# Kernel optimization log

Measured on AMD Instinct MI355X. Metric: run time of the kernel, lower is better.

## Reference

```python
import jax, jax.numpy as jnp
import numpy as np

NUM_CATEGORIES = 64
IN_DIM = 1024
OUT_DIM = 1024
BATCH = 32
SEQ = 512


def setup_inputs() -> dict:
    key = jax.random.key(0)
    k1, k2, k3 = jax.random.split(key, 3)
    x = jax.random.normal(k1, (BATCH, SEQ, IN_DIM), dtype=jnp.float32)
    category_ids = jax.random.randint(k2, (BATCH,), 0, NUM_CATEGORIES, dtype=jnp.int32)
    weight = (jax.random.normal(k3, (NUM_CATEGORIES, IN_DIM, OUT_DIM), dtype=jnp.float32) * 0.02)
    bias = jnp.zeros((NUM_CATEGORIES, OUT_DIM), dtype=jnp.float32)
    return {"x": x, "category_ids": category_ids, "weight": weight, "bias": bias}


def reference(x, category_ids, weight, bias):
    # Gather per-sample weights/biases: W [b, in, out], b [b, out]
    W = weight[category_ids]
    b = bias[category_ids]
    # x: [b, l, in] -> out: [b, l, out]
    return jnp.einsum('bli,bio->blo', x, W) + b[:, None, :]
```

## Files before the change

kernel.cpp:

```cpp
#include <hip/hip_runtime.h>
#include <type_traits>

#define NUM_CATEGORIES 64
#define IN_DIM 1024
#define OUT_DIM 1024
#define BATCH 32
#define SEQ 512

#define BM 256
#define BN 256
#define BK 32
#define NSTEP (IN_DIM / BK)

#define LDA 40
#define LDBW 260

typedef float f32x4 __attribute__((ext_vector_type(4)));
typedef float f32x2 __attribute__((ext_vector_type(2)));
typedef unsigned int u32x4 __attribute__((ext_vector_type(4)));
typedef __bf16 bf16x2 __attribute__((ext_vector_type(2)));
typedef __bf16 bf16x4 __attribute__((ext_vector_type(4)));
typedef __bf16 bf16x8 __attribute__((ext_vector_type(8)));

__global__ __launch_bounds__(512, 2)
void cslinear_kernel(const float* __restrict__ x,
                     const int* __restrict__ cid,
                     const float* __restrict__ weight,
                     const float* __restrict__ bias,
                     float* __restrict__ out) {
    __shared__ unsigned short As[2][BM * LDA];
    __shared__ unsigned int   Bs[2][(BK / 2) * LDBW];

    const int t    = threadIdx.x;
    const int lane = t & 63;
    const int w    = t >> 6;

    const int s    = blockIdx.x;
    const int xcd  = s & 7;
    const int ixd  = s >> 3;
    const int b    = xcd + 8 * (ixd >> 3);
    const int j    = ixd & 7;
    const int nt   = j & 3;
    const int mt   = j >> 2;

    const int c = cid[b];
    const float* Wp = weight + (size_t)c * IN_DIM * OUT_DIM + (size_t)nt * BN;
    const float* Xp = x + ((size_t)b * SEQ + (size_t)mt * BM) * IN_DIM;
    float* Op = out + ((size_t)b * SEQ + (size_t)mt * BM) * OUT_DIM + (size_t)nt * BN;

    f32x4 acc[8][4] = {};

    const int mbase = (w >> 2) * 128;
    const int nbase = (w & 3) * 64;
    const int lrow  = lane & 15;
    const int lhi   = lane >> 4;

    f32x4 ra[2][4];
    f32x4 rb0[2][2], rb1[2][2];

    auto LOAD_A = [&](int ks, auto S) {
        constexpr int ss = decltype(S)::value;
        const float* Xk = Xp + ks * BK;
        #pragma unroll
        for (int i = 0; i < 4; ++i) {
            int f   = i * 512 + t;
            int row = f >> 3;
            int c4  = f & 7;
            ra[ss][i] = *reinterpret_cast<const f32x4*>(Xk + (size_t)row * IN_DIM + c4 * 4);
        }
    };
    auto LOAD_B = [&](int ks, auto S) {
        constexpr int ss = decltype(S)::value;
        const float* Wk = Wp + (size_t)(ks * BK) * OUT_DIM;
        #pragma unroll
        for (int i = 0; i < 2; ++i) {
            int u  = i * 512 + t;
            int kp = u >> 6;
            int n4 = u & 63;
            const float* bse = Wk + (size_t)(2 * kp) * OUT_DIM + n4 * 4;
            rb0[ss][i] = *reinterpret_cast<const f32x4*>(bse);
            rb1[ss][i] = *reinterpret_cast<const f32x4*>(bse + OUT_DIM);
        }
    };

    auto ST_A = [&](auto S, auto I) {
        constexpr int ss = decltype(S)::value;
        constexpr int i  = decltype(I)::value;
        char* AsB = reinterpret_cast<char*>(&As[ss][0]);
        int f   = i * 512 + t;
        int row = f >> 3;
        int c4  = f & 7;
        bf16x4 a4 = __builtin_convertvector(ra[ss][i], bf16x4);
        *reinterpret_cast<bf16x4*>(AsB + row * (LDA * 2) + c4 * 8) = a4;
    };
    auto ST_B = [&](auto S, auto I) {
        constexpr int ss = decltype(S)::value;
        constexpr int i  = decltype(I)::value;
        unsigned int* BsW = &Bs[ss][0];
        int u  = i * 512 + t;
        int kp = u >> 6;
        int n4 = u & 63;
        u32x4 q;
        #pragma unroll
        for (int jj = 0; jj < 4; ++jj) {
            f32x2 pr;
            pr.x = rb0[ss][i][jj];
            pr.y = rb1[ss][i][jj];
            bf16x2 pb = __builtin_convertvector(pr, bf16x2);
            q[jj] = __builtin_bit_cast(unsigned int, pb);
        }
        *reinterpret_cast<u32x4*>(BsW + kp * LDBW + n4 * 4) = q;
    };

    constexpr std::integral_constant<int, 0> I0{};
    constexpr std::integral_constant<int, 1> I1{};
    constexpr std::integral_constant<int, 2> I2{};
    constexpr std::integral_constant<int, 3> I3{};
    constexpr std::integral_constant<int, 0> S0{};
    constexpr std::integral_constant<int, 1> S1{};

    auto CLUSTER = [&](auto S, auto Q, const bf16x8* bfr) {
        constexpr int ss = decltype(S)::value;
        constexpr int q  = decltype(Q)::value;
        const char* AsB = reinterpret_cast<const char*>(&As[ss][0]);
        __builtin_amdgcn_s_setprio(1);
        #pragma unroll
        for (int mi = q * 2; mi < q * 2 + 2; ++mi) {
            int r = mbase + mi * 16 + lrow;
            bf16x8 afr = *reinterpret_cast<const bf16x8*>(AsB + r * (LDA * 2) + lhi * 16);
            #pragma unroll
            for (int ni = 0; ni < 4; ++ni)
                acc[mi][ni] = __builtin_amdgcn_mfma_f32_16x16x32_bf16(
                    afr, bfr[ni], acc[mi][ni], 0, 0, 0);
        }
        __builtin_amdgcn_s_setprio(0);
    };

    auto REGION = [&](auto Sc, auto Sn, bool do_store, bool do_load, int ksl) {
        constexpr int sc = decltype(Sc)::value;
        const unsigned int* BsW = &Bs[sc][0];
        bf16x8 bfr[4];
        #pragma unroll
        for (int ni = 0; ni < 4; ++ni) {
            int n   = nbase + ni * 16 + lrow;
            int kp0 = lhi * 4;
            u32x4 wds;
            #pragma unroll
            for (int jj = 0; jj < 4; ++jj)
                wds[jj] = BsW[(kp0 + jj) * LDBW + n];
            bfr[ni] = __builtin_bit_cast(bf16x8, wds);
        }
        CLUSTER(Sc, I0, bfr);
        if (do_store) { ST_A(Sn, I0); ST_A(Sn, I1); }
        CLUSTER(Sc, I1, bfr);
        if (do_store) { ST_A(Sn, I2); ST_A(Sn, I3); }
        if (do_load)  LOAD_A(ksl, Sc);
        CLUSTER(Sc, I2, bfr);
        if (do_store) { ST_B(Sn, I0); }
        CLUSTER(Sc, I3, bfr);
        if (do_store) { ST_B(Sn, I1); }
        if (do_load)  LOAD_B(ksl, Sc);
    };

    LOAD_A(0, S0); LOAD_B(0, S0);
    ST_A(S0, I0); ST_A(S0, I1); ST_A(S0, I2); ST_A(S0, I3);
    ST_B(S0, I0); ST_B(S0, I1);
    LOAD_A(1, S1); LOAD_B(1, S1);
    asm volatile("s_waitcnt lgkmcnt(0)" ::: "memory");
    __builtin_amdgcn_s_barrier();

    for (int ks = 0; ks < NSTEP; ks += 2) {
        REGION(S0, S1, true, ks + 2 < NSTEP, ks + 2);
        asm volatile("s_waitcnt lgkmcnt(0)" ::: "memory");
        __builtin_amdgcn_s_barrier();

        REGION(S1, S0, ks + 2 < NSTEP, ks + 3 < NSTEP, ks + 3);
        if (ks + 2 < NSTEP) {
            asm volatile("s_waitcnt lgkmcnt(0)" ::: "memory");
            __builtin_amdgcn_s_barrier();
        }
    }

    const int lcol  = lane & 15;
    const int lrow4 = (lane >> 4) * 4;
    float bv[4];
    #pragma unroll
    for (int ni = 0; ni < 4; ++ni)
        bv[ni] = bias[(size_t)c * OUT_DIM + nt * BN + nbase + ni * 16 + lcol];

    #pragma unroll
    for (int mi = 0; mi < 8; ++mi) {
        int rbase = mbase + mi * 16 + lrow4;
        #pragma unroll
        for (int ni = 0; ni < 4; ++ni) {
            int ncol = nbase + ni * 16 + lcol;
            #pragma unroll
            for (int r = 0; r < 4; ++r) {
                Op[(size_t)(rbase + r) * OUT_DIM + ncol] = acc[mi][ni][r] + bv[ni];
            }
        }
    }
}

extern "C" void kernel_launch(void* const* d_in, const int* in_sizes, int n_in,
                              void* d_out, int out_size, void* d_ws, size_t ws_size,
                              hipStream_t stream) {
    const float* x      = (const float*)d_in[0];
    const int*   cid    = (const int*)d_in[1];
    const float* weight = (const float*)d_in[2];
    const float* bias   = (const float*)d_in[3];
    float* out = (float*)d_out;

    dim3 grid(256);
    dim3 block(512);
    hipLaunchKernelGGL(cslinear_kernel, grid, block, 0, stream,
                       x, cid, weight, bias, out);
}
```

Before: 53.42 us.

## Restructure K-step into two barrier-fenced half-tile phases with batched fragment reads

Replaces the four interleaved MFMA clusters per K-step with two phases, each reading four A fragments and issuing 16 MFMAs after a barrier and LDS wait. Global loads and LDS stores for the next buffer are grouped before each phase. The goal is to separate memory and compute phases across waves, ping-pong style, to improve overlap. In exchange it adds several extra workgroup barriers per K-step and more live fragment registers.

```diff
diff --git a/kernel.cpp b/kernel.cpp
--- a/kernel.cpp
+++ b/kernel.cpp
@@ -83,7 +83,7 @@
         }
     };
 
-    auto ST_A = [&](auto S, auto I) {
+    auto ST_A1 = [&](auto S, auto I) {
         constexpr int ss = decltype(S)::value;
         constexpr int i  = decltype(I)::value;
         char* AsB = reinterpret_cast<char*>(&As[ss][0]);
@@ -93,7 +93,7 @@
         bf16x4 a4 = __builtin_convertvector(ra[ss][i], bf16x4);
         *reinterpret_cast<bf16x4*>(AsB + row * (LDA * 2) + c4 * 8) = a4;
     };
-    auto ST_B = [&](auto S, auto I) {
+    auto ST_B1 = [&](auto S, auto I) {
         constexpr int ss = decltype(S)::value;
         constexpr int i  = decltype(I)::value;
         unsigned int* BsW = &Bs[ss][0];
@@ -112,34 +112,9 @@
         *reinterpret_cast<u32x4*>(BsW + kp * LDBW + n4 * 4) = q;
     };
 
-    constexpr std::integral_constant<int, 0> I0{};
-    constexpr std::integral_constant<int, 1> I1{};
-    constexpr std::integral_constant<int, 2> I2{};
-    constexpr std::integral_constant<int, 3> I3{};
-    constexpr std::integral_constant<int, 0> S0{};
-    constexpr std::integral_constant<int, 1> S1{};
-
-    auto CLUSTER = [&](auto S, auto Q, const bf16x8* bfr) {
-        constexpr int ss = decltype(S)::value;
-        constexpr int q  = decltype(Q)::value;
-        const char* AsB = reinterpret_cast<const char*>(&As[ss][0]);
-        __builtin_amdgcn_s_setprio(1);
-        #pragma unroll
-        for (int mi = q * 2; mi < q * 2 + 2; ++mi) {
-            int r = mbase + mi * 16 + lrow;
-            bf16x8 afr = *reinterpret_cast<const bf16x8*>(AsB + r * (LDA * 2) + lhi * 16);
-            #pragma unroll
-            for (int ni = 0; ni < 4; ++ni)
-                acc[mi][ni] = __builtin_amdgcn_mfma_f32_16x16x32_bf16(
-                    afr, bfr[ni], acc[mi][ni], 0, 0, 0);
-        }
-        __builtin_amdgcn_s_setprio(0);
-    };
-
-    auto REGION = [&](auto Sc, auto Sn, bool do_store, bool do_load, int ksl) {
-        constexpr int sc = decltype(Sc)::value;
-        const unsigned int* BsW = &Bs[sc][0];
-        bf16x8 bfr[4];
+    auto RD_B = [&](auto S, bf16x8* bfr) {
+        constexpr int ss = decltype(S)::value;
+        const unsigned int* BsW = &Bs[ss][0];
         #pragma unroll
         for (int ni = 0; ni < 4; ++ni) {
             int n   = nbase + ni * 16 + lrow;
@@ -150,35 +125,73 @@
                 wds[jj] = BsW[(kp0 + jj) * LDBW + n];
             bfr[ni] = __builtin_bit_cast(bf16x8, wds);
         }
-        CLUSTER(Sc, I0, bfr);
-        if (do_store) { ST_A(Sn, I0); ST_A(Sn, I1); }
-        CLUSTER(Sc, I1, bfr);
-        if (do_store) { ST_A(Sn, I2); ST_A(Sn, I3); }
+    };
+    auto RD_A = [&](auto S, int mih, bf16x8* afr) {
+        constexpr int ss = decltype(S)::value;
+        const char* AsB = reinterpret_cast<const char*>(&As[ss][0]);
+        #pragma unroll
+        for (int m2 = 0; m2 < 4; ++m2) {
+            int r = mbase + (mih * 4 + m2) * 16 + lrow;
+            afr[m2] = *reinterpret_cast<const bf16x8*>(AsB + r * (LDA * 2) + lhi * 16);
+        }
+    };
+    auto QUAD = [&](auto MIH, const bf16x8* afr, const bf16x8* bfr) {
+        constexpr int mih = decltype(MIH)::value;
+        __builtin_amdgcn_s_setprio(1);
+        #pragma unroll
+        for (int m2 = 0; m2 < 4; ++m2) {
+            #pragma unroll
+            for (int ni = 0; ni < 4; ++ni)
+                acc[mih * 4 + m2][ni] = __builtin_amdgcn_mfma_f32_16x16x32_bf16(
+                    afr[m2], bfr[ni], acc[mih * 4 + m2][ni], 0, 0, 0);
+        }
+        __builtin_amdgcn_s_setprio(0);
+    };
+
+    constexpr std::integral_constant<int, 0> I0{};
+    constexpr std::integral_constant<int, 1> I1{};
+    constexpr std::integral_constant<int, 2> I2{};
+    constexpr std::integral_constant<int, 3> I3{};
+    constexpr std::integral_constant<int, 0> M0{};
+    constexpr std::integral_constant<int, 1> M1{};
+    constexpr std::integral_constant<int, 0> S0{};
+    constexpr std::integral_constant<int, 1> S1{};
+
+    auto FENCE = [&]() {
+        __builtin_amdgcn_s_barrier();
+        asm volatile("s_waitcnt lgkmcnt(0)" ::: "memory");
+        __builtin_amdgcn_sched_barrier(0);
+    };
+
+    auto KSTEP = [&](auto Sc, auto Sn, bool do_store, bool do_load, int ksl) {
+        bf16x8 bfr[4], afr[4];
+
+        RD_B(Sc, bfr);
+        RD_A(Sc, 0, afr);
+        if (do_store) { ST_A1(Sn, I0); ST_A1(Sn, I1); ST_B1(Sn, I0); }
         if (do_load)  LOAD_A(ksl, Sc);
-        CLUSTER(Sc, I2, bfr);
-        if (do_store) { ST_B(Sn, I0); }
-        CLUSTER(Sc, I3, bfr);
-        if (do_store) { ST_B(Sn, I1); }
+        FENCE();
+        QUAD(M0, afr, bfr);
+        __builtin_amdgcn_s_barrier();
+
+        RD_A(Sc, 1, afr);
+        if (do_store) { ST_A1(Sn, I2); ST_A1(Sn, I3); ST_B1(Sn, I1); }
         if (do_load)  LOAD_B(ksl, Sc);
+        FENCE();
+        QUAD(M1, afr, bfr);
+        __builtin_amdgcn_s_barrier();
     };
 
     LOAD_A(0, S0); LOAD_B(0, S0);
-    ST_A(S0, I0); ST_A(S0, I1); ST_A(S0, I2); ST_A(S0, I3);
-    ST_B(S0, I0); ST_B(S0, I1);
+    ST_A1(S0, I0); ST_A1(S0, I1); ST_A1(S0, I2); ST_A1(S0, I3);
+    ST_B1(S0, I0); ST_B1(S0, I1);
     LOAD_A(1, S1); LOAD_B(1, S1);
     asm volatile("s_waitcnt lgkmcnt(0)" ::: "memory");
     __builtin_amdgcn_s_barrier();
 
     for (int ks = 0; ks < NSTEP; ks += 2) {
-        REGION(S0, S1, true, ks + 2 < NSTEP, ks + 2);
-        asm volatile("s_waitcnt lgkmcnt(0)" ::: "memory");
-        __builtin_amdgcn_s_barrier();
-
-        REGION(S1, S0, ks + 2 < NSTEP, ks + 3 < NSTEP, ks + 3);
-        if (ks + 2 < NSTEP) {
-            asm volatile("s_waitcnt lgkmcnt(0)" ::: "memory");
-            __builtin_amdgcn_s_barrier();
-        }
+        KSTEP(S0, S1, true, ks + 2 < NSTEP, ks + 2);
+        KSTEP(S1, S0, ks + 2 < NSTEP, ks + 3 < NSTEP, ks + 3);
     }
 
     const int lcol  = lane & 15;
```

After: 77.06 us. 1.44x slower.
